# Optimization experiments

Hardware: AMD Instinct MI355X
Metric: run time of the kernel (lower is better)

The kernel has to match this reference:

```python
import jax, jax.numpy as jnp
import numpy as np

DIM = 512
HEADS = 8
DIM_KEY = 32          # dim_key * heads * 2 == DIM (required by the module's own einsum)
NUM_EXPERTS = 65536
NUM_KEYS = 256        # sqrt(NUM_EXPERTS)
TOPK = 16             # product_key_topk == num_experts_per_head
BN_EPS = 1e-5         # flax BatchNorm eps; running stats at init => x / sqrt(1 + eps)


def setup_inputs() -> dict:
    key = jax.random.key(0)
    k1, k2, k3, k4, k5 = jax.random.split(key, 5)
    b, n = 2, 512
    x = jax.random.normal(k1, (b, n, DIM), dtype=jnp.float32)
    # Dense(dim_key*heads*2, use_bias=False): lecun-normal-ish scale
    w_q = jax.random.normal(k2, (DIM, DIM_KEY * HEADS * 2), dtype=jnp.float32) / np.sqrt(DIM)
    # params created with nn.initializers.normal() -> stddev 0.01
    keys = jax.random.normal(k3, (HEADS, NUM_KEYS, 2, DIM_KEY), dtype=jnp.float32) * 0.01
    weight_down_embed = jax.random.normal(k4, (NUM_EXPERTS, DIM), dtype=jnp.float32) * 0.01
    weight_up_embed = jax.random.normal(k5, (NUM_EXPERTS, DIM), dtype=jnp.float32) * 0.01
    return {"x": x, "w_q": w_q, "keys": keys,
            "weight_down_embed": weight_down_embed, "weight_up_embed": weight_up_embed}


def peer_forward(x, w_q, keys, weight_down_embed, weight_up_embed):
    b, n, _ = x.shape
    # to_queries: Dense (no bias) -> BatchNorm in eval mode with init running stats
    # (mean=0, var=1, scale=1, bias=0) -> pure rescale; Dropout(0.0) is identity.
    q = (x @ w_q) * (1.0 / np.sqrt(1.0 + BN_EPS))            # [b, n, DIM]
    # rearrange b n (p h d) -> p b n h d  with p=2
    queries = q.reshape(b, n, 2, HEADS, DIM_KEY).transpose(2, 0, 1, 3, 4)
    sim = jnp.einsum('pbnhd,hkpd->pbnhk', queries, keys)     # [2, b, n, h, NUM_KEYS]
    v0, i0 = jax.lax.top_k(sim[0], TOPK)
    v1, i1 = jax.lax.top_k(sim[1], TOPK)
    # NOTE: faithful to the source's tuple unpacking, which assigns
    # scores_x=v0 (values), scores_y=i0 (indices of axis 0); v1/i1 feed the
    # (unused) all_indices path. So the combined score is values0 + indices0.
    all_scores = v0[..., :, None] + i0[..., None, :].astype(v0.dtype)  # [b,n,h,TOPK,TOPK]
    all_scores = all_scores.reshape(*all_scores.shape[:-2], -1)        # [b,n,h,TOPK*TOPK]
    scores, pk_indices = jax.lax.top_k(all_scores, TOPK)               # [b,n,h,TOPK]
    # Faithful to source: gathers use pk_indices (positions in the TOPK^2 list),
    # NOT the remapped expert ids (`indices` is computed but never used).
    weights_down = jnp.take(weight_down_embed, pk_indices, axis=0)     # [b,n,h,k,DIM]
    weights_up = jnp.take(weight_up_embed, pk_indices, axis=0)         # [b,n,h,k,DIM]
    h = jnp.einsum('bnd,bnhkd->bnhk', q, weights_down)
    h = jax.nn.gelu(h)                                                 # approximate gelu (flax default)
    h = h * jax.nn.softmax(scores, axis=-1)
    out = jnp.einsum('bnhk,bnhkd->bnd', h, weights_up)                 # [b, n, DIM]
    return out


def reference(x, w_q, keys, weight_down_embed, weight_up_embed):
    return peer_forward(x, w_q, keys, weight_down_embed, weight_up_embed)
```

## Files before the change

### kernel.cpp

```cpp
#include <hip/hip_runtime.h>
#include <math.h>

#define DIM    512
#define HEADS  8
#define DK     32
#define NKEYS  256
#define PKTOP  16
#define NTOK   1024

template<int BM, int BN, int BK, int TM, int TN, bool BT>
__global__ __launch_bounds__(256)
void sgemm(const float* __restrict__ A, const float* __restrict__ B,
           float* __restrict__ C, int M, int N, int K, float scale)
{
    __shared__ float As[BK][BM + 4];
    __shared__ float Bs[BK][BN + 4];
    const int tid = threadIdx.x;
    const int tx  = tid & 15;
    const int ty  = tid >> 4;
    const int m0  = blockIdx.y * BM;
    const int n0  = blockIdx.x * BN;

    float acc[TM][TN];
#pragma unroll
    for (int i = 0; i < TM; ++i)
#pragma unroll
        for (int j = 0; j < TN; ++j) acc[i][j] = 0.f;

    for (int k0 = 0; k0 < K; k0 += BK) {
#pragma unroll
        for (int it = 0; it < (BM * BK / 4) / 256; ++it) {
            int L   = tid + 256 * it;
            int row = L / (BK / 4), kq = L % (BK / 4);
            float4 v = *(const float4*)(A + (size_t)(m0 + row) * K + k0 + kq * 4);
            As[kq * 4 + 0][row] = v.x; As[kq * 4 + 1][row] = v.y;
            As[kq * 4 + 2][row] = v.z; As[kq * 4 + 3][row] = v.w;
        }
        if (!BT) {
#pragma unroll
            for (int it = 0; it < (BK * BN / 4) / 256; ++it) {
                int L = tid + 256 * it;
                int k = L / (BN / 4), nq = L % (BN / 4);
                float4 v = *(const float4*)(B + (size_t)(k0 + k) * N + n0 + nq * 4);
                *(float4*)&Bs[k][nq * 4] = v;
            }
        } else {
#pragma unroll
            for (int it = 0; it < (BN * BK / 4) / 256; ++it) {
                int L = tid + 256 * it;
                int n = L / (BK / 4), kq = L % (BK / 4);
                float4 v = *(const float4*)(B + (size_t)(n0 + n) * K + k0 + kq * 4);
                Bs[kq * 4 + 0][n] = v.x; Bs[kq * 4 + 1][n] = v.y;
                Bs[kq * 4 + 2][n] = v.z; Bs[kq * 4 + 3][n] = v.w;
            }
        }
        __syncthreads();
#pragma unroll
        for (int k = 0; k < BK; ++k) {
            float a[TM], b[TN];
#pragma unroll
            for (int i = 0; i < TM; ++i) a[i] = As[k][ty * TM + i];
#pragma unroll
            for (int j = 0; j < TN; ++j) b[j] = Bs[k][tx * TN + j];
#pragma unroll
            for (int i = 0; i < TM; ++i)
#pragma unroll
                for (int j = 0; j < TN; ++j) acc[i][j] += a[i] * b[j];
        }
        __syncthreads();
    }
#pragma unroll
    for (int i = 0; i < TM; ++i)
#pragma unroll
        for (int j = 0; j < TN; ++j)
            C[(size_t)(m0 + ty * TM + i) * N + n0 + tx * TN + j] = acc[i][j] * scale;
}

__global__ __launch_bounds__(256)
void k_simtopk(const float* __restrict__ q, const float* __restrict__ keys,
               int* __restrict__ pk_out, float* __restrict__ wt_out)
{
    const int lane = threadIdx.x & 63;
    const int th   = blockIdx.x * 4 + (threadIdx.x >> 6);
    const int t    = th >> 3;
    const int hh   = th & 7;
    const int base = lane * 4;

    const float4* qv = (const float4*)(q + (size_t)t * DIM + hh * DK);
    float4 qr[8];
#pragma unroll
    for (int i = 0; i < 8; ++i) qr[i] = qv[i];

    float v1[4];
#pragma unroll
    for (int j = 0; j < 4; ++j) {
        int k = base + j;
        const float4* kv = (const float4*)(keys + ((size_t)hh * NKEYS + k) * 2 * DK);
        float s = 0.f;
#pragma unroll
        for (int i = 0; i < 8; ++i) {
            float4 kk = kv[i];
            s += kk.x * qr[i].x + kk.y * qr[i].y + kk.z * qr[i].z + kk.w * qr[i].w;
        }
        v1[j] = s;
    }

    float my_v0 = 0.f;
    int   my_i0[4] = {0, 0, 0, 0};
#pragma unroll
    for (int r = 0; r < 16; ++r) {
        float b = v1[0]; int bj = 0;
        if (v1[1] > b) { b = v1[1]; bj = 1; }
        if (v1[2] > b) { b = v1[2]; bj = 2; }
        if (v1[3] > b) { b = v1[3]; bj = 3; }
        float m = b;
#pragma unroll
        for (int off = 32; off; off >>= 1) m = fmaxf(m, __shfl_xor(m, off, 64));
        unsigned long long bal = __ballot(b == m);
        int wl   = __ffsll((long long)bal) - 1;
        int widx = __shfl(base + bj, wl, 64);
        if ((lane >> 2) == r)       my_v0        = m;
        if ((lane & 3) == (r >> 2)) my_i0[r & 3] = widx;
        if (lane == wl) v1[bj] = -INFINITY;
    }

    float v2[4];
#pragma unroll
    for (int jj = 0; jj < 4; ++jj) v2[jj] = my_v0 + (float)my_i0[jj];

    float sc0 = 0.f, ssum = 0.f, my_sc = 0.f;
    int   my_pk = 0;
#pragma unroll
    for (int r = 0; r < 16; ++r) {
        float b = v2[0]; int bj = 0;
        if (v2[1] > b) { b = v2[1]; bj = 1; }
        if (v2[2] > b) { b = v2[2]; bj = 2; }
        if (v2[3] > b) { b = v2[3]; bj = 3; }
        float m = b;
#pragma unroll
        for (int off = 32; off; off >>= 1) m = fmaxf(m, __shfl_xor(m, off, 64));
        unsigned long long bal = __ballot(b == m);
        int wl = __ffsll((long long)bal) - 1;
        int wc = __shfl(base + bj, wl, 64);
        if (r == 0) sc0 = m;
        ssum += expf(m - sc0);
        if (lane == r) { my_sc = m; my_pk = wc; }
        if (lane == wl) v2[bj] = -INFINITY;
    }
    if (lane < PKTOP) {
        int o = th * PKTOP + lane;
        pk_out[o] = my_pk;
        wt_out[o] = expf(my_sc - sc0) / ssum;
    }
}

__device__ __forceinline__ float gelu_t(float x)
{
    float x3 = x * x * x;
    return 0.5f * x * (1.f + tanhf(0.7978845608028654f * (x + 0.044715f * x3)));
}

#define GBM 32
#define GBN 32
#define GBK 64

__global__ __launch_bounds__(256)
void k_gemm_scatter(const float* __restrict__ A, const float* __restrict__ B,
                    const int* __restrict__ pk, const float* __restrict__ wt,
                    float* __restrict__ C)
{
    __shared__ float As[GBK][GBM + 4];
    __shared__ float Bs[GBK][GBN + 4];
    __shared__ float wsum[GBM][GBN + 1];
    const int tid = threadIdx.x;
    const int tx  = tid & 15;
    const int ty  = tid >> 4;
    const int m0  = blockIdx.y * GBM;
    const int n0  = blockIdx.x * GBN;

    for (int i = tid; i < GBM * (GBN + 1); i += 256)
        ((float*)wsum)[i] = 0.f;
    __syncthreads();
    for (int i = tid; i < GBM * 128; i += 256) {
        int tok = i >> 7, s = i & 127;
        int e = pk[(size_t)(m0 + tok) * 128 + s];
        if (e >= n0 && e < n0 + GBN)
            atomicAdd(&wsum[tok][e - n0], wt[(size_t)(m0 + tok) * 128 + s]);
    }

    float acc[2][2] = {{0.f, 0.f}, {0.f, 0.f}};
    const int K = DIM;
    for (int k0 = 0; k0 < K; k0 += GBK) {
#pragma unroll
        for (int it = 0; it < (GBM * GBK / 4) / 256; ++it) {
            int L   = tid + 256 * it;
            int row = L / (GBK / 4), kq = L % (GBK / 4);
            float4 v = *(const float4*)(A + (size_t)(m0 + row) * K + k0 + kq * 4);
            As[kq * 4 + 0][row] = v.x; As[kq * 4 + 1][row] = v.y;
            As[kq * 4 + 2][row] = v.z; As[kq * 4 + 3][row] = v.w;
        }
#pragma unroll
        for (int it = 0; it < (GBN * GBK / 4) / 256; ++it) {
            int L = tid + 256 * it;
            int n = L / (GBK / 4), kq = L % (GBK / 4);
            float4 v = *(const float4*)(B + (size_t)(n0 + n) * K + k0 + kq * 4);
            Bs[kq * 4 + 0][n] = v.x; Bs[kq * 4 + 1][n] = v.y;
            Bs[kq * 4 + 2][n] = v.z; Bs[kq * 4 + 3][n] = v.w;
        }
        __syncthreads();
#pragma unroll
        for (int k = 0; k < GBK; ++k) {
            float a0 = As[k][ty * 2], a1 = As[k][ty * 2 + 1];
            float b0 = Bs[k][tx * 2], b1 = Bs[k][tx * 2 + 1];
            acc[0][0] += a0 * b0; acc[0][1] += a0 * b1;
            acc[1][0] += a1 * b0; acc[1][1] += a1 * b1;
        }
        __syncthreads();
    }
#pragma unroll
    for (int i = 0; i < 2; ++i)
#pragma unroll
        for (int j = 0; j < 2; ++j) {
            int tok = ty * 2 + i, e = tx * 2 + j;
            C[(size_t)(m0 + tok) * NKEYS + n0 + e] =
                gelu_t(acc[i][j]) * wsum[tok][e];
        }
}

extern "C" void kernel_launch(void* const* d_in, const int* in_sizes, int n_in,
                              void* d_out, int out_size, void* d_ws, size_t ws_size,
                              hipStream_t stream)
{
    const float* x    = (const float*)d_in[0];
    const float* wq   = (const float*)d_in[1];
    const float* keys = (const float*)d_in[2];
    const float* wd   = (const float*)d_in[3];
    const float* wu   = (const float*)d_in[4];
    float* out = (float*)d_out;

    float* q  = (float*)d_ws;
    float* C  = q + NTOK * DIM;
    int*   pk = (int*)(C + NTOK * NKEYS);
    float* wt = (float*)(pk + NTOK * 128);

    const float bnscale = 1.0f / sqrtf(1.0f + 1e-5f);

    sgemm<32, 64, 64, 2, 4, false>
        <<<dim3(DIM / 64, NTOK / 32), 256, 0, stream>>>(x, wq, q, NTOK, DIM, DIM, bnscale);

    k_simtopk<<<dim3(NTOK * HEADS / 4), 256, 0, stream>>>(q, keys, pk, wt);

    k_gemm_scatter<<<dim3(NKEYS / GBN, NTOK / GBM), 256, 0, stream>>>(q, wd, pk, wt, C);

    sgemm<32, 64, 64, 2, 4, false>
        <<<dim3(DIM / 64, NTOK / 32), 256, 0, stream>>>(C, wu, out, NTOK, DIM, NKEYS, 1.0f);
}
```

Baseline: 334.1 us.

## Scatter top-k softmax weights via global atomics and use single-wave GEMM tiles

The top-k kernel now atomically adds each selected softmax weight straight into a dense per-token, per-key weight matrix. This replaces writing index and weight lists that the scatter GEMM later had to rescan with shared-memory atomics. The zeroing of that matrix is folded into the first GEMM, and all three GEMMs share one 64-thread kernel with 32x32 tiles, 4x4 register blocking and a fused gelu-times-weight epilogue. This adds global atomics and smaller workgroups, and the first GEMM's grid (512 blocks x 512 floats) exactly covers the 1024x256 weight matrix it zeroes.

```diff
diff --git a/kernel.cpp b/kernel.cpp
--- a/kernel.cpp
+++ b/kernel.cpp
@@ -8,77 +8,100 @@
 #define PKTOP  16
 #define NTOK   1024
 
-template<int BM, int BN, int BK, int TM, int TN, bool BT>
-__global__ __launch_bounds__(256)
-void sgemm(const float* __restrict__ A, const float* __restrict__ B,
-           float* __restrict__ C, int M, int N, int K, float scale)
-{
-    __shared__ float As[BK][BM + 4];
-    __shared__ float Bs[BK][BN + 4];
-    const int tid = threadIdx.x;
-    const int tx  = tid & 15;
-    const int ty  = tid >> 4;
-    const int m0  = blockIdx.y * BM;
-    const int n0  = blockIdx.x * BN;
-
-    float acc[TM][TN];
-#pragma unroll
-    for (int i = 0; i < TM; ++i)
-#pragma unroll
-        for (int j = 0; j < TN; ++j) acc[i][j] = 0.f;
-
-    for (int k0 = 0; k0 < K; k0 += BK) {
-#pragma unroll
-        for (int it = 0; it < (BM * BK / 4) / 256; ++it) {
-            int L   = tid + 256 * it;
-            int row = L / (BK / 4), kq = L % (BK / 4);
-            float4 v = *(const float4*)(A + (size_t)(m0 + row) * K + k0 + kq * 4);
-            As[kq * 4 + 0][row] = v.x; As[kq * 4 + 1][row] = v.y;
-            As[kq * 4 + 2][row] = v.z; As[kq * 4 + 3][row] = v.w;
+__device__ __forceinline__ float gelu_t(float x)
+{
+    float x3 = x * x * x;
+    return 0.5f * x * (1.f + tanhf(0.7978845608028654f * (x + 0.044715f * x3)));
+}
+
+template<bool BT, int EPI, bool ZW>
+__global__ __launch_bounds__(64)
+void wgemm(const float* __restrict__ A, const float* __restrict__ B,
+           float* __restrict__ C, int M, int N, int K, float scale,
+           float* __restrict__ WS)
+{
+    __shared__ float As[64][36];
+    __shared__ float Bs[64][36];
+    const int lane = threadIdx.x;
+    const int mg   = lane >> 3;
+    const int ng   = lane & 7;
+    const int m0   = blockIdx.y * 32;
+    const int n0   = blockIdx.x * 32;
+
+    if (ZW) {
+        const int bid = blockIdx.y * gridDim.x + blockIdx.x;
+        float4 z = make_float4(0.f, 0.f, 0.f, 0.f);
+        *(float4*)(WS + (size_t)bid * 512 + lane * 8)     = z;
+        *(float4*)(WS + (size_t)bid * 512 + lane * 8 + 4) = z;
+    }
+
+    const int r16 = lane >> 4;
+    const int c16 = lane & 15;
+    const int r8  = lane >> 3;
+    const int c8  = lane & 7;
+
+    float acc[4][4] = {{0.f}};
+
+    for (int k0 = 0; k0 < K; k0 += 64) {
+#pragma unroll
+        for (int it = 0; it < 8; ++it) {
+            int row  = r16 + 4 * it;
+            float4 v = *(const float4*)(A + (size_t)(m0 + row) * K + k0 + c16 * 4);
+            As[c16 * 4 + 0][row] = v.x; As[c16 * 4 + 1][row] = v.y;
+            As[c16 * 4 + 2][row] = v.z; As[c16 * 4 + 3][row] = v.w;
         }
         if (!BT) {
 #pragma unroll
-            for (int it = 0; it < (BK * BN / 4) / 256; ++it) {
-                int L = tid + 256 * it;
-                int k = L / (BN / 4), nq = L % (BN / 4);
-                float4 v = *(const float4*)(B + (size_t)(k0 + k) * N + n0 + nq * 4);
-                *(float4*)&Bs[k][nq * 4] = v;
+            for (int it = 0; it < 8; ++it) {
+                int kr   = r8 + 8 * it;
+                float4 v = *(const float4*)(B + (size_t)(k0 + kr) * N + n0 + c8 * 4);
+                *(float4*)&Bs[kr][c8 * 4] = v;
             }
         } else {
 #pragma unroll
-            for (int it = 0; it < (BN * BK / 4) / 256; ++it) {
-                int L = tid + 256 * it;
-                int n = L / (BK / 4), kq = L % (BK / 4);
-                float4 v = *(const float4*)(B + (size_t)(n0 + n) * K + k0 + kq * 4);
-                Bs[kq * 4 + 0][n] = v.x; Bs[kq * 4 + 1][n] = v.y;
-                Bs[kq * 4 + 2][n] = v.z; Bs[kq * 4 + 3][n] = v.w;
+            for (int it = 0; it < 8; ++it) {
+                int nr   = r16 + 4 * it;
+                float4 v = *(const float4*)(B + (size_t)(n0 + nr) * K + k0 + c16 * 4);
+                Bs[c16 * 4 + 0][nr] = v.x; Bs[c16 * 4 + 1][nr] = v.y;
+                Bs[c16 * 4 + 2][nr] = v.z; Bs[c16 * 4 + 3][nr] = v.w;
             }
         }
         __syncthreads();
 #pragma unroll
-        for (int k = 0; k < BK; ++k) {
-            float a[TM], b[TN];
-#pragma unroll
-            for (int i = 0; i < TM; ++i) a[i] = As[k][ty * TM + i];
-#pragma unroll
-            for (int j = 0; j < TN; ++j) b[j] = Bs[k][tx * TN + j];
-#pragma unroll
-            for (int i = 0; i < TM; ++i)
-#pragma unroll
-                for (int j = 0; j < TN; ++j) acc[i][j] += a[i] * b[j];
+        for (int k = 0; k < 64; ++k) {
+            float4 a = *(const float4*)&As[k][mg * 4];
+            float4 b = *(const float4*)&Bs[k][ng * 4];
+            float af[4] = {a.x, a.y, a.z, a.w};
+            float bf[4] = {b.x, b.y, b.z, b.w};
+#pragma unroll
+            for (int i = 0; i < 4; ++i)
+#pragma unroll
+                for (int j = 0; j < 4; ++j) acc[i][j] += af[i] * bf[j];
         }
         __syncthreads();
     }
-#pragma unroll
-    for (int i = 0; i < TM; ++i)
-#pragma unroll
-        for (int j = 0; j < TN; ++j)
-            C[(size_t)(m0 + ty * TM + i) * N + n0 + tx * TN + j] = acc[i][j] * scale;
+
+#pragma unroll
+    for (int i = 0; i < 4; ++i) {
+        int m = m0 + mg * 4 + i;
+        float4 o;
+        if (EPI == 1) {
+            float4 w = *(const float4*)(WS + (size_t)m * N + n0 + ng * 4);
+            o.x = gelu_t(acc[i][0]) * w.x;
+            o.y = gelu_t(acc[i][1]) * w.y;
+            o.z = gelu_t(acc[i][2]) * w.z;
+            o.w = gelu_t(acc[i][3]) * w.w;
+        } else {
+            o = make_float4(acc[i][0] * scale, acc[i][1] * scale,
+                            acc[i][2] * scale, acc[i][3] * scale);
+        }
+        *(float4*)(C + (size_t)m * N + n0 + ng * 4) = o;
+    }
 }
 
 __global__ __launch_bounds__(256)
 void k_simtopk(const float* __restrict__ q, const float* __restrict__ keys,
-               int* __restrict__ pk_out, float* __restrict__ wt_out)
+               float* __restrict__ wsum)
 {
     const int lane = threadIdx.x & 63;
     const int th   = blockIdx.x * 4 + (threadIdx.x >> 6);
@@ -147,84 +170,8 @@
         if (lane == r) { my_sc = m; my_pk = wc; }
         if (lane == wl) v2[bj] = -INFINITY;
     }
-    if (lane < PKTOP) {
-        int o = th * PKTOP + lane;
-        pk_out[o] = my_pk;
-        wt_out[o] = expf(my_sc - sc0) / ssum;
-    }
-}
-
-__device__ __forceinline__ float gelu_t(float x)
-{
-    float x3 = x * x * x;
-    return 0.5f * x * (1.f + tanhf(0.7978845608028654f * (x + 0.044715f * x3)));
-}
-
-#define GBM 32
-#define GBN 32
-#define GBK 64
-
-__global__ __launch_bounds__(256)
-void k_gemm_scatter(const float* __restrict__ A, const float* __restrict__ B,
-                    const int* __restrict__ pk, const float* __restrict__ wt,
-                    float* __restrict__ C)
-{
-    __shared__ float As[GBK][GBM + 4];
-    __shared__ float Bs[GBK][GBN + 4];
-    __shared__ float wsum[GBM][GBN + 1];
-    const int tid = threadIdx.x;
-    const int tx  = tid & 15;
-    const int ty  = tid >> 4;
-    const int m0  = blockIdx.y * GBM;
-    const int n0  = blockIdx.x * GBN;
-
-    for (int i = tid; i < GBM * (GBN + 1); i += 256)
-        ((float*)wsum)[i] = 0.f;
-    __syncthreads();
-    for (int i = tid; i < GBM * 128; i += 256) {
-        int tok = i >> 7, s = i & 127;
-        int e = pk[(size_t)(m0 + tok) * 128 + s];
-        if (e >= n0 && e < n0 + GBN)
-            atomicAdd(&wsum[tok][e - n0], wt[(size_t)(m0 + tok) * 128 + s]);
-    }
-
-    float acc[2][2] = {{0.f, 0.f}, {0.f, 0.f}};
-    const int K = DIM;
-    for (int k0 = 0; k0 < K; k0 += GBK) {
-#pragma unroll
-        for (int it = 0; it < (GBM * GBK / 4) / 256; ++it) {
-            int L   = tid + 256 * it;
-            int row = L / (GBK / 4), kq = L % (GBK / 4);
-            float4 v = *(const float4*)(A + (size_t)(m0 + row) * K + k0 + kq * 4);
-            As[kq * 4 + 0][row] = v.x; As[kq * 4 + 1][row] = v.y;
-            As[kq * 4 + 2][row] = v.z; As[kq * 4 + 3][row] = v.w;
-        }
-#pragma unroll
-        for (int it = 0; it < (GBN * GBK / 4) / 256; ++it) {
-            int L = tid + 256 * it;
-            int n = L / (GBK / 4), kq = L % (GBK / 4);
-            float4 v = *(const float4*)(B + (size_t)(n0 + n) * K + k0 + kq * 4);
-            Bs[kq * 4 + 0][n] = v.x; Bs[kq * 4 + 1][n] = v.y;
-            Bs[kq * 4 + 2][n] = v.z; Bs[kq * 4 + 3][n] = v.w;
-        }
-        __syncthreads();
-#pragma unroll
-        for (int k = 0; k < GBK; ++k) {
-            float a0 = As[k][ty * 2], a1 = As[k][ty * 2 + 1];
-            float b0 = Bs[k][tx * 2], b1 = Bs[k][tx * 2 + 1];
-            acc[0][0] += a0 * b0; acc[0][1] += a0 * b1;
-            acc[1][0] += a1 * b0; acc[1][1] += a1 * b1;
-        }
-        __syncthreads();
-    }
-#pragma unroll
-    for (int i = 0; i < 2; ++i)
-#pragma unroll
-        for (int j = 0; j < 2; ++j) {
-            int tok = ty * 2 + i, e = tx * 2 + j;
-            C[(size_t)(m0 + tok) * NKEYS + n0 + e] =
-                gelu_t(acc[i][j]) * wsum[tok][e];
-        }
+    if (lane < PKTOP)
+        atomicAdd(&wsum[(size_t)t * NKEYS + my_pk], expf(my_sc - sc0) / ssum);
 }
 
 extern "C" void kernel_launch(void* const* d_in, const int* in_sizes, int n_in,
@@ -238,20 +185,23 @@
     const float* wu   = (const float*)d_in[4];
     float* out = (float*)d_out;
 
-    float* q  = (float*)d_ws;
-    float* C  = q + NTOK * DIM;
-    int*   pk = (int*)(C + NTOK * NKEYS);
-    float* wt = (float*)(pk + NTOK * 128);
+    float* q    = (float*)d_ws;
+    float* Cb   = q + NTOK * DIM;
+    float* wsum = Cb + NTOK * NKEYS;
 
     const float bnscale = 1.0f / sqrtf(1.0f + 1e-5f);
 
-    sgemm<32, 64, 64, 2, 4, false>
-        <<<dim3(DIM / 64, NTOK / 32), 256, 0, stream>>>(x, wq, q, NTOK, DIM, DIM, bnscale);
-
-    k_simtopk<<<dim3(NTOK * HEADS / 4), 256, 0, stream>>>(q, keys, pk, wt);
-
-    k_gemm_scatter<<<dim3(NKEYS / GBN, NTOK / GBM), 256, 0, stream>>>(q, wd, pk, wt, C);
-
-    sgemm<32, 64, 64, 2, 4, false>
-        <<<dim3(DIM / 64, NTOK / 32), 256, 0, stream>>>(C, wu, out, NTOK, DIM, NKEYS, 1.0f);
-}
+    wgemm<false, 0, true>
+        <<<dim3(DIM / 32, NTOK / 32), 64, 0, stream>>>(x, wq, q, NTOK, DIM, DIM,
+                                                       bnscale, wsum);
+
+    k_simtopk<<<dim3(NTOK * HEADS / 4), 256, 0, stream>>>(q, keys, wsum);
+
+    wgemm<true, 1, false>
+        <<<dim3(NKEYS / 32, NTOK / 32), 64, 0, stream>>>(q, wd, Cb, NTOK, NKEYS,
+                                                         DIM, 1.f, wsum);
+
+    wgemm<false, 0, false>
+        <<<dim3(DIM / 32, NTOK / 32), 64, 0, stream>>>(Cb, wu, out, NTOK, DIM,
+                                                       NKEYS, 1.f, (float*)nullptr);
+}
```

After: 338.7 us. Within noise of the previous version (+1.4%).

## Replace iterative top-k with radix-select and scatter softmax weights via global atomics

Applied to the files above, without the earlier changes.

The 16-round argmax top-k loops are replaced by a bitwise radix threshold selection using ballots, followed by a small shared-memory rank sort for the first top-k. The second stage computes softmax weights and atomically accumulates them straight into a dense per-token wsum buffer. That buffer is zeroed by the first GEMM, so the separate gemm_scatter kernel with its per-block pk scan disappears and the generic sgemm gets a gelu*wsum epilogue. Tie-breaking and float atomic ordering may differ slightly from the reference.

```diff
diff --git a/kernel.cpp b/kernel.cpp
--- a/kernel.cpp
+++ b/kernel.cpp
@@ -8,10 +8,17 @@
 #define PKTOP  16
 #define NTOK   1024
 
-template<int BM, int BN, int BK, int TM, int TN, bool BT>
+__device__ __forceinline__ float gelu_t(float x)
+{
+    float x3 = x * x * x;
+    return 0.5f * x * (1.f + tanhf(0.7978845608028654f * (x + 0.044715f * x3)));
+}
+
+template<int BM, int BN, int BK, int TM, int TN, bool BT, int EPI, bool ZW>
 __global__ __launch_bounds__(256)
 void sgemm(const float* __restrict__ A, const float* __restrict__ B,
-           float* __restrict__ C, int M, int N, int K, float scale)
+           float* __restrict__ C, int M, int N, int K, float scale,
+           float* __restrict__ WS)
 {
     __shared__ float As[BK][BM + 4];
     __shared__ float Bs[BK][BN + 4];
@@ -21,6 +28,11 @@
     const int m0  = blockIdx.y * BM;
     const int n0  = blockIdx.x * BN;
 
+    if (ZW) {
+        const int bid = blockIdx.y * gridDim.x + blockIdx.x;
+        *(float4*)(WS + (size_t)bid * 1024 + tid * 4) = make_float4(0.f, 0.f, 0.f, 0.f);
+    }
+
     float acc[TM][TN];
 #pragma unroll
     for (int i = 0; i < TM; ++i)
@@ -70,18 +82,71 @@
         __syncthreads();
     }
 #pragma unroll
-    for (int i = 0; i < TM; ++i)
-#pragma unroll
-        for (int j = 0; j < TN; ++j)
-            C[(size_t)(m0 + ty * TM + i) * N + n0 + tx * TN + j] = acc[i][j] * scale;
+    for (int i = 0; i < TM; ++i) {
+        int m = m0 + ty * TM + i;
+#pragma unroll
+        for (int j = 0; j < TN; ++j) {
+            int n = n0 + tx * TN + j;
+            if (EPI == 1)
+                C[(size_t)m * N + n] = gelu_t(acc[i][j]) * WS[(size_t)m * N + n];
+            else
+                C[(size_t)m * N + n] = acc[i][j] * scale;
+        }
+    }
+}
+
+__device__ __forceinline__ unsigned f2mono(float f)
+{
+    int b = __float_as_int(f);
+    return (unsigned)(b ^ ((b >> 31) | 0x80000000));
+}
+__device__ __forceinline__ int mbcnt64(unsigned long long m)
+{
+    return __builtin_amdgcn_mbcnt_hi((unsigned)(m >> 32),
+           __builtin_amdgcn_mbcnt_lo((unsigned)m, 0));
+}
+
+__device__ __forceinline__ void select_top16(const unsigned u[4], bool sel[4])
+{
+    unsigned tau = 0;
+    for (int bit = 31; bit >= 0; --bit) {
+        unsigned t = tau | (1u << bit);
+        int cnt = 0;
+#pragma unroll
+        for (int j = 0; j < 4; ++j)
+            cnt += __popcll(__ballot(u[j] >= t));
+        if (cnt >= 16) tau = t;
+    }
+    bool gt[4], eq[4];
+    int n_gt = 0, below = 0;
+#pragma unroll
+    for (int j = 0; j < 4; ++j) {
+        gt[j] = (u[j] > tau);
+        eq[j] = (u[j] == tau);
+        n_gt  += __popcll(__ballot(gt[j]));
+        below += mbcnt64(__ballot(eq[j]));
+    }
+    const int need = 16 - n_gt;
+    int run = 0;
+#pragma unroll
+    for (int j = 0; j < 4; ++j) {
+        sel[j] = gt[j] || (eq[j] && (below + run) < need);
+        run += eq[j] ? 1 : 0;
+    }
 }
 
 __global__ __launch_bounds__(256)
 void k_simtopk(const float* __restrict__ q, const float* __restrict__ keys,
-               int* __restrict__ pk_out, float* __restrict__ wt_out)
-{
+               float* __restrict__ wsum)
+{
+    __shared__ float Sv[4][16];
+    __shared__ int   Sc[4][16];
+    __shared__ float V0[4][16];
+    __shared__ int   I0[4][16];
+
+    const int wid  = threadIdx.x >> 6;
     const int lane = threadIdx.x & 63;
-    const int th   = blockIdx.x * 4 + (threadIdx.x >> 6);
+    const int th   = blockIdx.x * 4 + wid;
     const int t    = th >> 3;
     const int hh   = th & 7;
     const int base = lane * 4;
@@ -94,8 +159,7 @@
     float v1[4];
 #pragma unroll
     for (int j = 0; j < 4; ++j) {
-        int k = base + j;
-        const float4* kv = (const float4*)(keys + ((size_t)hh * NKEYS + k) * 2 * DK);
+        const float4* kv = (const float4*)(keys + ((size_t)hh * NKEYS + base + j) * 2 * DK);
         float s = 0.f;
 #pragma unroll
         for (int i = 0; i < 8; ++i) {
@@ -105,126 +169,68 @@
         v1[j] = s;
     }
 
-    float my_v0 = 0.f;
-    int   my_i0[4] = {0, 0, 0, 0};
-#pragma unroll
-    for (int r = 0; r < 16; ++r) {
-        float b = v1[0]; int bj = 0;
-        if (v1[1] > b) { b = v1[1]; bj = 1; }
-        if (v1[2] > b) { b = v1[2]; bj = 2; }
-        if (v1[3] > b) { b = v1[3]; bj = 3; }
-        float m = b;
-#pragma unroll
-        for (int off = 32; off; off >>= 1) m = fmaxf(m, __shfl_xor(m, off, 64));
-        unsigned long long bal = __ballot(b == m);
-        int wl   = __ffsll((long long)bal) - 1;
-        int widx = __shfl(base + bj, wl, 64);
-        if ((lane >> 2) == r)       my_v0        = m;
-        if ((lane & 3) == (r >> 2)) my_i0[r & 3] = widx;
-        if (lane == wl) v1[bj] = -INFINITY;
-    }
-
-    float v2[4];
-#pragma unroll
-    for (int jj = 0; jj < 4; ++jj) v2[jj] = my_v0 + (float)my_i0[jj];
-
-    float sc0 = 0.f, ssum = 0.f, my_sc = 0.f;
-    int   my_pk = 0;
-#pragma unroll
-    for (int r = 0; r < 16; ++r) {
-        float b = v2[0]; int bj = 0;
-        if (v2[1] > b) { b = v2[1]; bj = 1; }
-        if (v2[2] > b) { b = v2[2]; bj = 2; }
-        if (v2[3] > b) { b = v2[3]; bj = 3; }
-        float m = b;
-#pragma unroll
-        for (int off = 32; off; off >>= 1) m = fmaxf(m, __shfl_xor(m, off, 64));
-        unsigned long long bal = __ballot(b == m);
-        int wl = __ffsll((long long)bal) - 1;
-        int wc = __shfl(base + bj, wl, 64);
-        if (r == 0) sc0 = m;
-        ssum += expf(m - sc0);
-        if (lane == r) { my_sc = m; my_pk = wc; }
-        if (lane == wl) v2[bj] = -INFINITY;
-    }
-    if (lane < PKTOP) {
-        int o = th * PKTOP + lane;
-        pk_out[o] = my_pk;
-        wt_out[o] = expf(my_sc - sc0) / ssum;
-    }
-}
-
-__device__ __forceinline__ float gelu_t(float x)
-{
-    float x3 = x * x * x;
-    return 0.5f * x * (1.f + tanhf(0.7978845608028654f * (x + 0.044715f * x3)));
-}
-
-#define GBM 32
-#define GBN 32
-#define GBK 64
-
-__global__ __launch_bounds__(256)
-void k_gemm_scatter(const float* __restrict__ A, const float* __restrict__ B,
-                    const int* __restrict__ pk, const float* __restrict__ wt,
-                    float* __restrict__ C)
-{
-    __shared__ float As[GBK][GBM + 4];
-    __shared__ float Bs[GBK][GBN + 4];
-    __shared__ float wsum[GBM][GBN + 1];
-    const int tid = threadIdx.x;
-    const int tx  = tid & 15;
-    const int ty  = tid >> 4;
-    const int m0  = blockIdx.y * GBM;
-    const int n0  = blockIdx.x * GBN;
-
-    for (int i = tid; i < GBM * (GBN + 1); i += 256)
-        ((float*)wsum)[i] = 0.f;
+    unsigned u1[4];
+#pragma unroll
+    for (int j = 0; j < 4; ++j) u1[j] = f2mono(v1[j]);
+    bool sel1[4];
+    select_top16(u1, sel1);
+
+    int below = 0;
+#pragma unroll
+    for (int j = 0; j < 4; ++j) below += mbcnt64(__ballot(sel1[j]));
+    int run = 0;
+#pragma unroll
+    for (int j = 0; j < 4; ++j) {
+        if (sel1[j]) { Sv[wid][below + run] = v1[j]; Sc[wid][below + run] = base + j; }
+        run += sel1[j] ? 1 : 0;
+    }
     __syncthreads();
-    for (int i = tid; i < GBM * 128; i += 256) {
-        int tok = i >> 7, s = i & 127;
-        int e = pk[(size_t)(m0 + tok) * 128 + s];
-        if (e >= n0 && e < n0 + GBN)
-            atomicAdd(&wsum[tok][e - n0], wt[(size_t)(m0 + tok) * 128 + s]);
-    }
-
-    float acc[2][2] = {{0.f, 0.f}, {0.f, 0.f}};
-    const int K = DIM;
-    for (int k0 = 0; k0 < K; k0 += GBK) {
-#pragma unroll
-        for (int it = 0; it < (GBM * GBK / 4) / 256; ++it) {
-            int L   = tid + 256 * it;
-            int row = L / (GBK / 4), kq = L % (GBK / 4);
-            float4 v = *(const float4*)(A + (size_t)(m0 + row) * K + k0 + kq * 4);
-            As[kq * 4 + 0][row] = v.x; As[kq * 4 + 1][row] = v.y;
-            As[kq * 4 + 2][row] = v.z; As[kq * 4 + 3][row] = v.w;
-        }
-#pragma unroll
-        for (int it = 0; it < (GBN * GBK / 4) / 256; ++it) {
-            int L = tid + 256 * it;
-            int n = L / (GBK / 4), kq = L % (GBK / 4);
-            float4 v = *(const float4*)(B + (size_t)(n0 + n) * K + k0 + kq * 4);
-            Bs[kq * 4 + 0][n] = v.x; Bs[kq * 4 + 1][n] = v.y;
-            Bs[kq * 4 + 2][n] = v.z; Bs[kq * 4 + 3][n] = v.w;
-        }
-        __syncthreads();
-#pragma unroll
-        for (int k = 0; k < GBK; ++k) {
-            float a0 = As[k][ty * 2], a1 = As[k][ty * 2 + 1];
-            float b0 = Bs[k][tx * 2], b1 = Bs[k][tx * 2 + 1];
-            acc[0][0] += a0 * b0; acc[0][1] += a0 * b1;
-            acc[1][0] += a1 * b0; acc[1][1] += a1 * b1;
-        }
-        __syncthreads();
-    }
-#pragma unroll
-    for (int i = 0; i < 2; ++i)
-#pragma unroll
-        for (int j = 0; j < 2; ++j) {
-            int tok = ty * 2 + i, e = tx * 2 + j;
-            C[(size_t)(m0 + tok) * NKEYS + n0 + e] =
-                gelu_t(acc[i][j]) * wsum[tok][e];
-        }
+
+    {
+        float mv = Sv[wid][lane & 15];
+        int   mc = Sc[wid][lane & 15];
+        int rank = 0;
+#pragma unroll
+        for (int k = 0; k < 16; ++k) {
+            float ov = Sv[wid][k];
+            int   oc = Sc[wid][k];
+            rank += (ov > mv || (ov == mv && oc < mc)) ? 1 : 0;
+        }
+        if (lane < 16) { V0[wid][rank] = mv; I0[wid][rank] = mc; }
+    }
+    __syncthreads();
+
+    const float v0v = V0[wid][lane >> 2];
+    const int4  iv  = *(const int4*)&I0[wid][(lane & 3) * 4];
+    float f[4];
+    f[0] = v0v + (float)iv.x; f[1] = v0v + (float)iv.y;
+    f[2] = v0v + (float)iv.z; f[3] = v0v + (float)iv.w;
+    unsigned u2[4];
+#pragma unroll
+    for (int j = 0; j < 4; ++j) u2[j] = f2mono(f[j]);
+    bool sel2[4];
+    select_top16(u2, sel2);
+
+    int mi = max(max(iv.x, iv.y), max(iv.z, iv.w));
+    mi = max(mi, __shfl_xor(mi, 1, 64));
+    mi = max(mi, __shfl_xor(mi, 2, 64));
+    const float mx = V0[wid][0] + (float)mi;
+
+    float e[4];
+    float s = 0.f;
+#pragma unroll
+    for (int j = 0; j < 4; ++j) {
+        e[j] = sel2[j] ? expf(f[j] - mx) : 0.f;
+        s += e[j];
+    }
+#pragma unroll
+    for (int off = 32; off; off >>= 1) s += __shfl_xor(s, off, 64);
+    const float inv = 1.f / s;
+
+#pragma unroll
+    for (int j = 0; j < 4; ++j)
+        if (sel2[j])
+            atomicAdd(&wsum[(size_t)t * NKEYS + base + j], e[j] * inv);
 }
 
 extern "C" void kernel_launch(void* const* d_in, const int* in_sizes, int n_in,
@@ -238,20 +244,23 @@
     const float* wu   = (const float*)d_in[4];
     float* out = (float*)d_out;
 
-    float* q  = (float*)d_ws;
-    float* C  = q + NTOK * DIM;
-    int*   pk = (int*)(C + NTOK * NKEYS);
-    float* wt = (float*)(pk + NTOK * 128);
+    float* q    = (float*)d_ws;
+    float* Cb   = q + NTOK * DIM;
+    float* wsum = Cb + NTOK * NKEYS;
 
     const float bnscale = 1.0f / sqrtf(1.0f + 1e-5f);
 
-    sgemm<32, 64, 64, 2, 4, false>
-        <<<dim3(DIM / 64, NTOK / 32), 256, 0, stream>>>(x, wq, q, NTOK, DIM, DIM, bnscale);
-
-    k_simtopk<<<dim3(NTOK * HEADS / 4), 256, 0, stream>>>(q, keys, pk, wt);
-
-    k_gemm_scatter<<<dim3(NKEYS / GBN, NTOK / GBM), 256, 0, stream>>>(q, wd, pk, wt, C);
-
-    sgemm<32, 64, 64, 2, 4, false>
-        <<<dim3(DIM / 64, NTOK / 32), 256, 0, stream>>>(C, wu, out, NTOK, DIM, NKEYS, 1.0f);
-}
+    sgemm<32, 64, 64, 2, 4, false, 0, true>
+        <<<dim3(DIM / 64, NTOK / 32), 256, 0, stream>>>(x, wq, q, NTOK, DIM, DIM,
+                                                        bnscale, wsum);
+
+    k_simtopk<<<dim3(NTOK * HEADS / 4), 256, 0, stream>>>(q, keys, wsum);
+
+    sgemm<32, 32, 64, 2, 2, true, 1, false>
+        <<<dim3(NKEYS / 32, NTOK / 32), 256, 0, stream>>>(q, wd, Cb, NTOK, NKEYS,
+                                                          DIM, 1.f, wsum);
+
+    sgemm<32, 64, 64, 2, 4, false, 0, false>
+        <<<dim3(DIM / 64, NTOK / 32), 256, 0, stream>>>(Cb, wu, out, NTOK, DIM,
+                                                        NKEYS, 1.f, wsum);
+}
```

Measured after the change: 322.4 us. -3.5%, faster.
